# Performance work log

Hardware: AMD Instinct MI355X
Metric: run time of the kernel (lower is better)

## Reference

```python
import jax, jax.numpy as jnp
import numpy as np

B, T, C = 1, 2048, 1024
H = 16
HD = C // H  # 64
K = 8
EPS = 1e-6
NEG = -1.0e9


def apply_rotary_emb(x, cos, sin):
    # x: (B,T,H,HD), cos/sin: (T, HD//2)
    x1, x2 = jnp.split(x, 2, axis=-1)
    c = cos[None, :, None, :]
    s = sin[None, :, None, :]
    return jnp.concatenate([x1 * c - x2 * s, x1 * s + x2 * c], axis=-1)


def rms_norm(x):
    return x * jax.lax.rsqrt(jnp.mean(jnp.square(x), axis=-1, keepdims=True) + EPS)


def setup_inputs() -> dict:
    key = jax.random.key(0)
    ks = jax.random.split(key, 8)
    x = jax.random.normal(ks[0], (B, T, C), dtype=jnp.float32)
    # standard RoPE tables
    inv_freq = 1.0 / (10000.0 ** (np.arange(0, HD, 2, dtype=np.float32) / HD))
    t = np.arange(T, dtype=np.float32)
    freqs = np.outer(t, inv_freq)  # (T, HD//2)
    cos = jnp.asarray(np.cos(freqs), dtype=jnp.float32)
    sin = jnp.asarray(np.sin(freqs), dtype=jnp.float32)
    std = 0.02
    Wq = std * jax.random.normal(ks[1], (C, C), dtype=jnp.float32)
    Wk = std * jax.random.normal(ks[2], (C, C), dtype=jnp.float32)
    Wv = std * jax.random.normal(ks[3], (C, C), dtype=jnp.float32)
    Wproj = std * jax.random.normal(ks[4], (C, C), dtype=jnp.float32)
    Wdq = jax.random.normal(ks[5], (C, K), dtype=jnp.float32) / np.sqrt(C)
    Wdk = jax.random.normal(ks[6], (C, K), dtype=jnp.float32) / np.sqrt(C)
    return {"x": x, "cos": cos, "sin": sin, "Wq": Wq, "Wk": Wk, "Wv": Wv,
            "Wproj": Wproj, "Wdq": Wdq, "Wdk": Wdk}


def reference(x, cos, sin, Wq, Wk, Wv, Wproj, Wdq, Wdk):
    b, t, c = x.shape
    q = (x @ Wq).reshape(b, t, H, HD)
    k = (x @ Wk).reshape(b, t, H, HD)
    v = (x @ Wv).reshape(b, t, H, HD)
    q = rms_norm(apply_rotary_emb(q, cos, sin))
    k = rms_norm(apply_rotary_emb(k, cos, sin))

    # digit projections (identical for every head in the source module)
    qd = x @ Wdq  # (B,T,K)
    kd = x @ Wdk  # (B,T,K)
    matches = qd[:, :, None, :] == kd[:, None, :, :]  # (B,Tq,Tk,K)
    prefix = jnp.cumprod(matches.astype(jnp.int32), axis=-1)
    lcp = jnp.sum(prefix, axis=-1)  # (B,Tq,Tk)
    lcp_mask = lcp >= (K - 1)

    causal = jnp.tril(jnp.ones((t, t), dtype=bool))
    combined = causal[None, None, :, :] & lcp_mask[:, None, :, :]  # (B,1->H,Tq,Tk)

    scale = 1.0 / jnp.sqrt(jnp.asarray(HD, x.dtype))
    scores = jnp.einsum('bqhd,bkhd->bhqk', q * scale, k)
    scores = jnp.where(combined, scores, NEG)
    w = jax.nn.softmax(scores, axis=-1)
    y = jnp.einsum('bhqk,bkhd->bqhd', w, v).reshape(b, t, c)
    return y @ Wproj
```

## Files before the change

kernel.cpp:

```cpp
#include <hip/hip_runtime.h>
#include <math.h>

#define T_DIM 2048
#define C_DIM 1024
#define H_NUM 16
#define HD_DIM 64
#define K_LCP 8
#define NEG_VAL -1.0e9f

typedef __bf16 bf16;
typedef __bf16 bf16x4 __attribute__((ext_vector_type(4)));
typedef __bf16 bf16x8 __attribute__((ext_vector_type(8)));
typedef float f32x4 __attribute__((ext_vector_type(4)));

__device__ void matvec_body(const float* __restrict__ vin, int npart,
                            const float* __restrict__ W, float* __restrict__ vout,
                            float scale, int blk) {
  __shared__ float xm[C_DIM];
  __shared__ float red[4][64];
  const int t = threadIdx.x;
  f32x4 s = {0.f, 0.f, 0.f, 0.f};
  if (npart) {
    for (int g = 0; g < npart; ++g) s += ((const f32x4*)vin)[g * 256 + t];
  } else {
    s = ((const f32x4*)vin)[t];
  }
  s *= scale;
  *(f32x4*)&xm[t * 4] = s;
  __syncthreads();
  const int j = blk * 64 + (t & 63);
  const int p = t >> 6;
  float acc = 0.f;
  for (int c = p * 256; c < p * 256 + 256; ++c)
    acc = fmaf(xm[c], W[(size_t)c * C_DIM + j], acc);
  red[p][t & 63] = acc;
  __syncthreads();
  if (t < 64)
    vout[blk * 64 + t] = (red[0][t] + red[1][t]) + (red[2][t] + red[3][t]);
}

__global__ __launch_bounds__(256) void fused_a(const float* __restrict__ x,
                                               const float* __restrict__ Wdq,
                                               const float* __restrict__ Wdk,
                                               bf16* __restrict__ xb,
                                               float* __restrict__ qd,
                                               float* __restrict__ kd,
                                               float* __restrict__ partial,
                                               int* __restrict__ flags) {
  const int tid = threadIdx.x;
  if (blockIdx.x >= 512) {
    const int b = blockIdx.x - 512;
    if (b == 0 && tid < 116) flags[tid] = 0;
    f32x4 s = {0.f, 0.f, 0.f, 0.f};
    for (int r = 0; r < 64; ++r)
      s += ((const f32x4*)(x + (size_t)(b * 64 + r) * C_DIM))[tid];
    ((f32x4*)(partial + (size_t)b * C_DIM))[tid] = s;
    return;
  }
  const int wave = tid >> 6, lane = tid & 63;
  const int t = blockIdx.x * 4 + wave;
  const float* xp = x + (size_t)t * C_DIM;
  bf16* xbp = xb + (size_t)t * C_DIM;
  float aq[8] = {}, ak[8] = {};
#pragma unroll
  for (int i = 0; i < 16; ++i) {
    const int c = i * 64 + lane;
    float xv = xp[c];
    xbp[c] = (bf16)xv;
    float4 wq0 = *(const float4*)(Wdq + (size_t)c * K_LCP);
    float4 wq1 = *(const float4*)(Wdq + (size_t)c * K_LCP + 4);
    float4 wk0 = *(const float4*)(Wdk + (size_t)c * K_LCP);
    float4 wk1 = *(const float4*)(Wdk + (size_t)c * K_LCP + 4);
    aq[0] = fmaf(xv, wq0.x, aq[0]); aq[1] = fmaf(xv, wq0.y, aq[1]);
    aq[2] = fmaf(xv, wq0.z, aq[2]); aq[3] = fmaf(xv, wq0.w, aq[3]);
    aq[4] = fmaf(xv, wq1.x, aq[4]); aq[5] = fmaf(xv, wq1.y, aq[5]);
    aq[6] = fmaf(xv, wq1.z, aq[6]); aq[7] = fmaf(xv, wq1.w, aq[7]);
    ak[0] = fmaf(xv, wk0.x, ak[0]); ak[1] = fmaf(xv, wk0.y, ak[1]);
    ak[2] = fmaf(xv, wk0.z, ak[2]); ak[3] = fmaf(xv, wk0.w, ak[3]);
    ak[4] = fmaf(xv, wk1.x, ak[4]); ak[5] = fmaf(xv, wk1.y, ak[5]);
    ak[6] = fmaf(xv, wk1.z, ak[6]); ak[7] = fmaf(xv, wk1.w, ak[7]);
  }
#pragma unroll
  for (int j = 0; j < 8; ++j) {
#pragma unroll
    for (int off = 32; off >= 1; off >>= 1) {
      aq[j] += __shfl_xor(aq[j], off);
      ak[j] += __shfl_xor(ak[j], off);
    }
  }
  if (lane == 0) {
    *(float4*)(qd + (size_t)t * K_LCP) = make_float4(aq[0], aq[1], aq[2], aq[3]);
    *(float4*)(qd + (size_t)t * K_LCP + 4) = make_float4(aq[4], aq[5], aq[6], aq[7]);
    *(float4*)(kd + (size_t)t * K_LCP) = make_float4(ak[0], ak[1], ak[2], ak[3]);
    *(float4*)(kd + (size_t)t * K_LCP + 4) = make_float4(ak[4], ak[5], ak[6], ak[7]);
  }
}

__global__ __launch_bounds__(256) void fused_b(
    const float* __restrict__ qd, const float* __restrict__ kd,
    const float* __restrict__ partial, const float* __restrict__ Wv,
    int* __restrict__ tilemask, int* __restrict__ allmask,
    float* __restrict__ vmean, int* __restrict__ qneed, int* __restrict__ kneed,
    int* __restrict__ vneed, int* __restrict__ vtneed, int* __restrict__ pneed,
    int* __restrict__ wneed) {
  const int tid = threadIdx.x;
  if (blockIdx.x >= 128) {
    matvec_body(partial, 32, Wv, vmean, 1.0f / 2048.0f, blockIdx.x - 128);
    return;
  }
  const int qb = blockIdx.x;
  __shared__ float qds[16][K_LCP];
  __shared__ int tm[32];
  if (tid < 32) tm[tid] = 0;
  if (tid < 16 * K_LCP)
    qds[tid >> 3][tid & 7] = qd[(size_t)(qb * 16 + (tid >> 3)) * K_LCP + (tid & 7)];
  __syncthreads();
  for (int key = tid; key < T_DIM; key += 256) {
    float kv[K_LCP];
    *(float4*)&kv[0] = *(const float4*)(kd + (size_t)key * K_LCP);
    *(float4*)&kv[4] = *(const float4*)(kd + (size_t)key * K_LCP + 4);
    int any = 0;
#pragma unroll
    for (int ql = 0; ql < 16; ++ql) {
      int qg = qb * 16 + ql;
      if (key > qg) continue;
      int lcp = 0;
#pragma unroll
      for (int jj = 0; jj < K_LCP; ++jj) {
        if (qds[ql][jj] == kv[jj]) lcp++;
        else break;
      }
      if (lcp >= K_LCP - 1) any = 1;
    }
    if (any) tm[key >> 6] = 1;
  }
  __syncthreads();
  int anytm = 0;
#pragma unroll
  for (int i = 0; i < 32; ++i) anytm |= tm[i];
  if (tid < 32) tilemask[qb * 32 + tid] = tm[tid];
  if (tid == 0) allmask[qb] = !anytm;
  if (anytm) {
    if (tid < 32) {
      if (tm[tid]) {
        atomicOr(&kneed[tid >> 1], 1);
        atomicOr(&vneed[tid >> 1], 1);
      } else {
        atomicOr(&vtneed[tid], 1);
        atomicOr(&vneed[tid >> 1], 1);
      }
    }
    if (tid == 0) {
      atomicOr(&qneed[qb >> 3], 1);
      atomicOr(&pneed[qb >> 2], 1);
      atomicOr(&wneed[0], 1);
      atomicOr(&wneed[1], 1);
      atomicOr(&wneed[2], 1);
      atomicOr(&wneed[3], 1);
    }
  }
}

__global__ __launch_bounds__(256) void fused_e(
    const float* __restrict__ vmean, const float* __restrict__ WprojF,
    float* __restrict__ rowout, const float* __restrict__ W0,
    const float* __restrict__ W1, const float* __restrict__ W2,
    const float* __restrict__ W3, bf16* __restrict__ O0, bf16* __restrict__ O1,
    bf16* __restrict__ O2, bf16* __restrict__ O3, const int* __restrict__ wneed) {
  if (blockIdx.x < 16) {
    matvec_body(vmean, 0, WprojF, rowout, 1.0f, blockIdx.x);
    return;
  }
  const int idx = blockIdx.x - 16;
  const int z = idx >> 8;
  if (!wneed[z]) return;
  const float* W = (z == 0) ? W0 : (z == 1) ? W1 : (z == 2) ? W2 : W3;
  bf16* O = (z == 0) ? O0 : (z == 1) ? O1 : (z == 2) ? O2 : O3;
  __shared__ bf16 tile[64][65];
  const int rem = idx & 255;
  const int bk = (rem >> 4) * 64;
  const int bn = (rem & 15) * 64;
  const int r = threadIdx.x >> 2;
  const int c0 = (threadIdx.x & 3) * 16;
  const float* src = W + (size_t)(bk + r) * C_DIM + bn + c0;
#pragma unroll
  for (int t = 0; t < 16; t += 4) {
    float4 f = *(const float4*)(src + t);
    tile[r][c0 + t + 0] = (bf16)f.x;
    tile[r][c0 + t + 1] = (bf16)f.y;
    tile[r][c0 + t + 2] = (bf16)f.z;
    tile[r][c0 + t + 3] = (bf16)f.w;
  }
  __syncthreads();
  bf16* dst = O + (size_t)(bn + r) * C_DIM + bk + c0;
#pragma unroll
  for (int t = 0; t < 16; ++t) dst[t] = tile[c0 + t][r];
}

template <int TMt, int MI, int NA>
__global__ __launch_bounds__(256) void gemm_bf16(
    const bf16* __restrict__ A, const bf16* __restrict__ Bt0,
    const bf16* __restrict__ Bt1, const bf16* __restrict__ Bt2, void* C0,
    void* C1, void* C2, int N, int Kd, int bf16_out,
    const float* __restrict__ cosT, const float* __restrict__ sinT,
    const int* __restrict__ fq, const int* __restrict__ fk,
    const int* __restrict__ fv, float* __restrict__ vtsum,
    const float* __restrict__ rowout, int mode) {
  if (!mode && blockIdx.z == 1) {
    const int b = blockIdx.y * 8 + blockIdx.x;
    f32x4 v = ((const f32x4*)rowout)[threadIdx.x];
#pragma unroll
    for (int r = 0; r < 8; ++r) {
      const int row = b * 8 + r;
      if (fq[row >> 6]) continue;
      ((f32x4*)((float*)C0 + (size_t)row * C_DIM))[threadIdx.x] = v;
    }
    return;
  }
  if (mode) {
    const int* f = (blockIdx.z == 0) ? fq : (blockIdx.z == 1) ? fk : fv;
    if (!f[blockIdx.y]) return;
  } else {
    if (!fq[blockIdx.y]) return;
  }
  const bf16* Bt = (blockIdx.z == 0) ? Bt0 : (blockIdx.z == 1) ? Bt1 : Bt2;
  __shared__ __align__(16) bf16 As[TMt * 32];
  __shared__ __align__(16) bf16 Bs[128 * 32];
  const int tid = threadIdx.x;
  const int bm = blockIdx.y * TMt;
  const int bn = blockIdx.x * 128;
  const int wave = tid >> 6, lane = tid & 63;
  const int lr = lane >> 2;
  const int lc = (lane & 3) * 8;
  bf16* gA = (bf16*)(A + (size_t)(bm + wave * 16 * NA + lr) * Kd + lc);
  bf16* gB = (bf16*)(Bt + (size_t)(bn + wave * 32 + lr) * Kd + lc);
  bf16* lA = As + wave * 512 * NA;
  bf16* lB = Bs + wave * 1024;
  const int wr = (wave >> 1) * (MI * 16);
  const int wc = (wave & 1) * 64;
  const int fm = lane & 15;
  const int fk_ = (lane >> 4) * 8;

  f32x4 acc[MI][4] = {};
  for (int k0 = 0; k0 < Kd; k0 += 32) {
    __syncthreads();
#pragma unroll
    for (int u = 0; u < NA; ++u)
      __builtin_amdgcn_global_load_lds(
          (__attribute__((address_space(1))) void*)(gA + (size_t)u * 16 * Kd + k0),
          (__attribute__((address_space(3))) void*)(lA + u * 512), 16, 0, 0);
#pragma unroll
    for (int u = 0; u < 2; ++u)
      __builtin_amdgcn_global_load_lds(
          (__attribute__((address_space(1))) void*)(gB + (size_t)u * 16 * Kd + k0),
          (__attribute__((address_space(3))) void*)(lB + u * 512), 16, 0, 0);
    __syncthreads();
    bf16x8 af[MI], bfr[4];
#pragma unroll
    for (int i = 0; i < MI; ++i)
      af[i] = *(const bf16x8*)(As + (size_t)(wr + i * 16 + fm) * 32 + fk_);
#pragma unroll
    for (int j = 0; j < 4; ++j)
      bfr[j] = *(const bf16x8*)(Bs + (size_t)(wc + j * 16 + fm) * 32 + fk_);
#pragma unroll
    for (int i = 0; i < MI; ++i)
#pragma unroll
      for (int j = 0; j < 4; ++j)
        acc[i][j] = __builtin_amdgcn_mfma_f32_16x16x32_bf16(af[i], bfr[j],
                                                            acc[i][j], 0, 0, 0);
  }
  const int cq = (lane >> 4) * 4;
  if (mode && blockIdx.z < 2) {
    bf16* C = (bf16*)((blockIdx.z == 0) ? C0 : C1);
#pragma unroll
    for (int i = 0; i < MI; ++i)
#pragma unroll
      for (int r = 0; r < 4; ++r) {
        const int t = bm + wr + i * 16 + cq + r;
        float c0 = cosT[(size_t)t * 32 + fm], s0 = sinT[(size_t)t * 32 + fm];
        float c1 = cosT[(size_t)t * 32 + 16 + fm], s1 = sinT[(size_t)t * 32 + 16 + fm];
        float a0 = acc[i][0][r], a1 = acc[i][1][r];
        float a2 = acc[i][2][r], a3 = acc[i][3][r];
        float o0 = a0 * c0 - a2 * s0, o2 = a0 * s0 + a2 * c0;
        float o1 = a1 * c1 - a3 * s1, o3 = a1 * s1 + a3 * c1;
        float ss = o0 * o0 + o1 * o1 + o2 * o2 + o3 * o3;
        ss += __shfl_xor(ss, 1);
        ss += __shfl_xor(ss, 2);
        ss += __shfl_xor(ss, 4);
        ss += __shfl_xor(ss, 8);
        float rn = 1.0f / sqrtf(ss * (1.0f / 64.0f) + 1e-6f);
        size_t base = (size_t)t * N + bn + wc + fm;
        C[base + 0] = (bf16)(o0 * rn);
        C[base + 16] = (bf16)(o1 * rn);
        C[base + 32] = (bf16)(o2 * rn);
        C[base + 48] = (bf16)(o3 * rn);
      }
  } else if (bf16_out) {
    bf16* C = (bf16*)((blockIdx.z == 0) ? C0 : (blockIdx.z == 1) ? C1 : C2);
#pragma unroll
    for (int i = 0; i < MI; ++i)
#pragma unroll
      for (int r = 0; r < 4; ++r) {
        size_t base = (size_t)(bm + wr + i * 16 + cq + r) * N + bn + wc + fm;
#pragma unroll
        for (int j = 0; j < 4; ++j) C[base + j * 16] = (bf16)acc[i][j][r];
      }
    if (mode && blockIdx.z == 2 && MI == 4) {
      const int kt = (bm + wr) >> 6;
#pragma unroll
      for (int j = 0; j < 4; ++j) {
        float s = 0.f;
#pragma unroll
        for (int i = 0; i < MI; ++i)
#pragma unroll
          for (int r = 0; r < 4; ++r) s += acc[i][j][r];
        s += __shfl_xor(s, 16);
        s += __shfl_xor(s, 32);
        if ((lane >> 4) == 0)
          vtsum[(size_t)kt * C_DIM + bn + wc + j * 16 + fm] = s;
      }
    }
  } else {
    float* C = (float*)((blockIdx.z == 0) ? C0 : (blockIdx.z == 1) ? C1 : C2);
#pragma unroll
    for (int i = 0; i < MI; ++i)
#pragma unroll
      for (int r = 0; r < 4; ++r) {
        size_t base = (size_t)(bm + wr + i * 16 + cq + r) * N + bn + wc + fm;
#pragma unroll
        for (int j = 0; j < 4; ++j) C[base + j * 16] = acc[i][j][r];
      }
  }
}

#define QT 16
#define KT 64

__global__ __launch_bounds__(256) void attn2(
    const bf16* __restrict__ q, const bf16* __restrict__ k,
    const bf16* __restrict__ v, const float* __restrict__ qd,
    const float* __restrict__ kd, const float* __restrict__ vtsum,
    const float* __restrict__ vmean, const int* __restrict__ tilemask,
    const int* __restrict__ allmask, const int* __restrict__ pneed,
    bf16* __restrict__ y) {
  const int h = blockIdx.y;
  const int qb = blockIdx.x;
  const int q0 = qb * QT;
  const int tid = threadIdx.x;
  const int q_l = tid >> 4;
  const int sub = tid & 15;

  if (allmask[qb]) {
    if (pneed[qb >> 2]) {
      f32x4 vm = *(const f32x4*)(vmean + h * HD_DIM + sub * 4);
      bf16x4 o = {(bf16)vm[0], (bf16)vm[1], (bf16)vm[2], (bf16)vm[3]};
      *(bf16x4*)(y + (size_t)(q0 + q_l) * C_DIM + h * HD_DIM + sub * 4) = o;
    }
    return;
  }

  __shared__ float qs[QT][HD_DIM];
  __shared__ float qds[QT][K_LCP];
  __shared__ float ks[KT][HD_DIM];
  __shared__ float vs[KT][HD_DIM];
  __shared__ float kds[KT][K_LCP];
  __shared__ float sc[QT][KT + 4];

  {
    int r = tid >> 4, c4 = (tid & 15) * 4;
    bf16x4 t4 = *(const bf16x4*)(q + (size_t)(q0 + r) * C_DIM + h * HD_DIM + c4);
    qs[r][c4 + 0] = (float)t4[0] * 0.125f;
    qs[r][c4 + 1] = (float)t4[1] * 0.125f;
    qs[r][c4 + 2] = (float)t4[2] * 0.125f;
    qs[r][c4 + 3] = (float)t4[3] * 0.125f;
    if (tid < QT * K_LCP)
      qds[tid >> 3][tid & 7] = qd[(size_t)(q0 + (tid >> 3)) * K_LCP + (tid & 7)];
  }
  __syncthreads();

  float m = -INFINITY;
  float l = 0.f;
  float acc[4] = {0.f, 0.f, 0.f, 0.f};

  for (int kt = 0; kt < T_DIM / KT; ++kt) {
    if (!tilemask[qb * 32 + kt]) {
      if (m <= NEG_VAL) {
        m = NEG_VAL;
        l += (float)KT;
        f32x4 vt = *(const f32x4*)(vtsum + (size_t)kt * C_DIM + h * HD_DIM + sub * 4);
        acc[0] += vt[0];
        acc[1] += vt[1];
        acc[2] += vt[2];
        acc[3] += vt[3];
      }
      continue;
    }
    const int k0 = kt * KT;
    __syncthreads();
#pragma unroll
    for (int it = 0; it < 4; ++it) {
      int i = tid + it * 256;
      int row = i >> 4, c4 = (i & 15) * 4;
      bf16x4 kv = *(const bf16x4*)(k + (size_t)(k0 + row) * C_DIM + h * HD_DIM + c4);
      bf16x4 vv = *(const bf16x4*)(v + (size_t)(k0 + row) * C_DIM + h * HD_DIM + c4);
      ks[row][c4 + 0] = (float)kv[0];
      ks[row][c4 + 1] = (float)kv[1];
      ks[row][c4 + 2] = (float)kv[2];
      ks[row][c4 + 3] = (float)kv[3];
      vs[row][c4 + 0] = (float)vv[0];
      vs[row][c4 + 1] = (float)vv[1];
      vs[row][c4 + 2] = (float)vv[2];
      vs[row][c4 + 3] = (float)vv[3];
    }
#pragma unroll
    for (int it = 0; it < 2; ++it) {
      int i = tid + it * 256;
      kds[i >> 3][i & 7] = kd[(size_t)(k0 + (i >> 3)) * K_LCP + (i & 7)];
    }
    __syncthreads();

    const int kb = sub * 4;
    bool msk[4];
#pragma unroll
    for (int j = 0; j < 4; ++j) {
      int kg = k0 + kb + j;
      int lcp = 0;
#pragma unroll
      for (int jj = 0; jj < K_LCP; ++jj) {
        if (qds[q_l][jj] == kds[kb + j][jj]) lcp++;
        else break;
      }
      msk[j] = (lcp >= K_LCP - 1) && (kg <= q0 + q_l);
    }
    float s[4] = {0.f, 0.f, 0.f, 0.f};
#pragma unroll
    for (int d4 = 0; d4 < 16; ++d4) {
      float4 q4 = *(const float4*)&qs[q_l][d4 * 4];
#pragma unroll
      for (int j = 0; j < 4; ++j) {
        float4 k4 = *(const float4*)&ks[kb + j][d4 * 4];
        s[j] = fmaf(q4.x, k4.x, s[j]);
        s[j] = fmaf(q4.y, k4.y, s[j]);
        s[j] = fmaf(q4.z, k4.z, s[j]);
        s[j] = fmaf(q4.w, k4.w, s[j]);
      }
    }
    float tmax = NEG_VAL;
#pragma unroll
    for (int j = 0; j < 4; ++j) {
      s[j] = msk[j] ? s[j] : NEG_VAL;
      tmax = fmaxf(tmax, s[j]);
    }
#pragma unroll
    for (int off = 1; off < 16; off <<= 1) tmax = fmaxf(tmax, __shfl_xor(tmax, off));
    float m_new = fmaxf(m, tmax);
    float alpha = expf(m - m_new);
    float lsum = 0.f;
#pragma unroll
    for (int j = 0; j < 4; ++j) {
      float p = expf(s[j] - m_new);
      sc[q_l][kb + j] = p;
      lsum += p;
    }
#pragma unroll
    for (int off = 1; off < 16; off <<= 1) lsum += __shfl_xor(lsum, off);
    l = l * alpha + lsum;
    m = m_new;
    acc[0] *= alpha;
    acc[1] *= alpha;
    acc[2] *= alpha;
    acc[3] *= alpha;
    __syncthreads();
#pragma unroll 8
    for (int kk = 0; kk < KT; ++kk) {
      float w = sc[q_l][kk];
      const float4 v4 = *(const float4*)&vs[kk][sub * 4];
      acc[0] = fmaf(w, v4.x, acc[0]);
      acc[1] = fmaf(w, v4.y, acc[1]);
      acc[2] = fmaf(w, v4.z, acc[2]);
      acc[3] = fmaf(w, v4.w, acc[3]);
    }
  }

  const float inv_l = 1.0f / l;
  bf16x4 o = {(bf16)(acc[0] * inv_l), (bf16)(acc[1] * inv_l),
              (bf16)(acc[2] * inv_l), (bf16)(acc[3] * inv_l)};
  *(bf16x4*)(y + (size_t)(q0 + q_l) * C_DIM + h * HD_DIM + sub * 4) = o;
}

extern "C" void kernel_launch(void* const* d_in, const int* in_sizes, int n_in,
                              void* d_out, int out_size, void* d_ws, size_t ws_size,
                              hipStream_t stream) {
  const float* x = (const float*)d_in[0];
  const float* cosT = (const float*)d_in[1];
  const float* sinT = (const float*)d_in[2];
  const float* Wq = (const float*)d_in[3];
  const float* Wk = (const float*)d_in[4];
  const float* Wv = (const float*)d_in[5];
  const float* Wproj = (const float*)d_in[6];
  const float* Wdq = (const float*)d_in[7];
  const float* Wdk = (const float*)d_in[8];
  float* out = (float*)d_out;

  char* ws = (char*)d_ws;
  const size_t TC2 = (size_t)T_DIM * C_DIM * 2;
  const size_t CC2 = (size_t)C_DIM * C_DIM * 2;
  bf16* xb = (bf16*)(ws + 0);
  bf16* wqt = (bf16*)(ws + TC2);
  bf16* wkt = (bf16*)(ws + TC2 + CC2);
  bf16* wvt = (bf16*)(ws + TC2 + 2 * CC2);
  bf16* wpt = (bf16*)(ws + TC2 + 3 * CC2);
  bf16* qb = (bf16*)(ws + TC2 + 4 * CC2);
  bf16* kb = (bf16*)(ws + 2 * TC2 + 4 * CC2);
  bf16* vb = (bf16*)(ws + 3 * TC2 + 4 * CC2);
  char* p2 = ws + 4 * TC2 + 4 * CC2;
  float* qd = (float*)p2;                      p2 += (size_t)T_DIM * K_LCP * 4;
  float* kd = (float*)p2;                      p2 += (size_t)T_DIM * K_LCP * 4;
  float* vtsum = (float*)p2;                   p2 += 32 * C_DIM * 4;
  float* vmean = (float*)p2;                   p2 += C_DIM * 4;
  float* partial = (float*)p2;                 p2 += 32 * C_DIM * 4;
  float* rowout = (float*)p2;                  p2 += C_DIM * 4;
  int* tilemask = (int*)p2;                    p2 += (T_DIM / 16) * 32 * 4;
  int* allmask = (int*)p2;                     p2 += (T_DIM / 16) * 4;
  int* qneed = (int*)p2;                       p2 += 16 * 4;
  int* kneed = (int*)p2;                       p2 += 16 * 4;
  int* vneed = (int*)p2;                       p2 += 16 * 4;
  int* vtneed = (int*)p2;                      p2 += 32 * 4;
  int* pneed = (int*)p2;                       p2 += 32 * 4;
  int* wneed = (int*)p2;                       p2 += 4 * 4;
  bf16* yb = xb;

  fused_a<<<544, 256, 0, stream>>>(x, Wdq, Wdk, xb, qd, kd, partial, qneed);
  fused_b<<<144, 256, 0, stream>>>(qd, kd, partial, Wv, tilemask, allmask,
                                   vmean, qneed, kneed, vneed, vtneed, pneed,
                                   wneed);
  fused_e<<<16 + 1024, 256, 0, stream>>>(vmean, Wproj, rowout, Wq, Wk, Wv,
                                         Wproj, wqt, wkt, wvt, wpt, wneed);
  gemm_bf16<128, 4, 2><<<dim3(C_DIM / 128, T_DIM / 128, 3), 256, 0, stream>>>(
      xb, wqt, wkt, wvt, qb, kb, vb, C_DIM, C_DIM, 1, cosT, sinT, qneed, kneed,
      vneed, vtsum, rowout, 1);
  attn2<<<dim3(T_DIM / QT, H_NUM), 256, 0, stream>>>(
      qb, kb, vb, qd, kd, vtsum, vmean, tilemask, allmask, pneed, yb);
  gemm_bf16<64, 2, 1><<<dim3(C_DIM / 128, T_DIM / 64, 2), 256, 0, stream>>>(
      yb, wpt, wpt, wpt, out, out, out, C_DIM, C_DIM, 0, cosT, sinT, pneed,
      pneed, pneed, vtsum, rowout, 0);
}
```

Before: 121.6 us.

## Fuse all stages into one persistent kernel with grid-wide barriers

Replaces six separate kernel launches with a single persistent kernel of 256 blocks. Each stage runs as a grid-stride loop over virtual blocks, and the stages are separated by a custom atomic-based grid barrier. Shared memory is unified through a union. The goal is to remove launch overhead and inter-kernel gaps. The weight transposes are now always performed, where before they were gated by the wneed flags. In exchange it risks deadlock if not all blocks are co-resident, adds barrier spin cost, and reduces parallelism in stages that previously used many more blocks (1040, 2048).

```diff
diff --git a/kernel.cpp b/kernel.cpp
--- a/kernel.cpp
+++ b/kernel.cpp
@@ -7,70 +7,72 @@
 #define HD_DIM 64
 #define K_LCP 8
 #define NEG_VAL -1.0e9f
+#define SYNC_MAGIC 0x13579BDF
 
 typedef __bf16 bf16;
 typedef __bf16 bf16x4 __attribute__((ext_vector_type(4)));
 typedef __bf16 bf16x8 __attribute__((ext_vector_type(8)));
 typedef float f32x4 __attribute__((ext_vector_type(4)));
 
-__device__ void matvec_body(const float* __restrict__ vin, int npart,
-                            const float* __restrict__ W, float* __restrict__ vout,
-                            float scale, int blk) {
-  __shared__ float xm[C_DIM];
-  __shared__ float red[4][64];
-  const int t = threadIdx.x;
-  f32x4 s = {0.f, 0.f, 0.f, 0.f};
-  if (npart) {
-    for (int g = 0; g < npart; ++g) s += ((const f32x4*)vin)[g * 256 + t];
-  } else {
-    s = ((const f32x4*)vin)[t];
-  }
-  s *= scale;
-  *(f32x4*)&xm[t * 4] = s;
-  __syncthreads();
-  const int j = blk * 64 + (t & 63);
-  const int p = t >> 6;
-  float acc = 0.f;
-  for (int c = p * 256; c < p * 256 + 256; ++c)
-    acc = fmaf(xm[c], W[(size_t)c * C_DIM + j], acc);
-  red[p][t & 63] = acc;
-  __syncthreads();
-  if (t < 64)
-    vout[blk * 64 + t] = (red[0][t] + red[1][t]) + (red[2][t] + red[3][t]);
-}
-
-__global__ __launch_bounds__(256) void fused_a(const float* __restrict__ x,
-                                               const float* __restrict__ Wdq,
-                                               const float* __restrict__ Wdk,
-                                               bf16* __restrict__ xb,
-                                               float* __restrict__ qd,
-                                               float* __restrict__ kd,
-                                               float* __restrict__ partial,
-                                               int* __restrict__ flags) {
-  const int tid = threadIdx.x;
-  if (blockIdx.x >= 512) {
-    const int b = blockIdx.x - 512;
-    if (b == 0 && tid < 116) flags[tid] = 0;
-    f32x4 s = {0.f, 0.f, 0.f, 0.f};
-    for (int r = 0; r < 64; ++r)
-      s += ((const f32x4*)(x + (size_t)(b * 64 + r) * C_DIM))[tid];
-    ((f32x4*)(partial + (size_t)b * C_DIM))[tid] = s;
-    return;
-  }
-  const int wave = tid >> 6, lane = tid & 63;
-  const int t = blockIdx.x * 4 + wave;
-  const float* xp = x + (size_t)t * C_DIM;
-  bf16* xbp = xb + (size_t)t * C_DIM;
+struct Args {
+  const float *x, *cosT, *sinT, *Wq, *Wk, *Wv, *Wproj, *Wdq, *Wdk;
+  float* out;
+  bf16 *xb, *wqt, *wkt, *wvt, *wpt, *qB, *kB, *vB;
+  float *qd, *kd, *vtsum, *vmean, *partial, *rowout;
+  int *tilemask, *allmask, *qneed, *kneed, *vneed, *vtneed, *pneed;
+  int* sync;
+};
+
+union SmemU {
+  struct {
+    float qs[16][64]; float qds[16][8]; float ks[64][64]; float vs[64][64];
+    float kds[64][8]; float sc[16][68];
+  } attn;
+  struct { bf16 As[128 * 32]; bf16 Bs[128 * 32]; } gemm;
+  struct { bf16 tile[64][65]; } tp;
+  struct { float xm[C_DIM]; float red[4][64]; } mv;
+  struct { float qds[16][8]; int tm[32]; } tmask;
+};
+
+__device__ void gsync(int* s, int nb) {
+  __syncthreads();
+  if (threadIdx.x == 0) {
+    __threadfence();
+    int g = __hip_atomic_load(&s[2], __ATOMIC_RELAXED, __HIP_MEMORY_SCOPE_AGENT);
+    int old = __hip_atomic_fetch_add(&s[1], 1, __ATOMIC_ACQ_REL,
+                                     __HIP_MEMORY_SCOPE_AGENT);
+    if (old == nb - 1) {
+      __hip_atomic_store(&s[1], 0, __ATOMIC_RELAXED, __HIP_MEMORY_SCOPE_AGENT);
+      __hip_atomic_store(&s[2], g + 1, __ATOMIC_RELEASE,
+                         __HIP_MEMORY_SCOPE_AGENT);
+    } else {
+      int it = 0;
+      while (__hip_atomic_load(&s[2], __ATOMIC_ACQUIRE,
+                               __HIP_MEMORY_SCOPE_AGENT) == g) {
+        __builtin_amdgcn_s_sleep(2);
+        if (++it > (1 << 25)) break;
+      }
+    }
+    __threadfence();
+  }
+  __syncthreads();
+}
+
+__device__ void conv_qdkd_body(const Args& a, int vb) {
+  const int wave = threadIdx.x >> 6, lane = threadIdx.x & 63;
+  const int t = vb * 4 + wave;
+  const float* xp = a.x + (size_t)t * C_DIM;
+  bf16* xbp = a.xb + (size_t)t * C_DIM;
   float aq[8] = {}, ak[8] = {};
 #pragma unroll
   for (int i = 0; i < 16; ++i) {
     const int c = i * 64 + lane;
     float xv = xp[c];
     xbp[c] = (bf16)xv;
-    float4 wq0 = *(const float4*)(Wdq + (size_t)c * K_LCP);
-    float4 wq1 = *(const float4*)(Wdq + (size_t)c * K_LCP + 4);
-    float4 wk0 = *(const float4*)(Wdk + (size_t)c * K_LCP);
-    float4 wk1 = *(const float4*)(Wdk + (size_t)c * K_LCP + 4);
+    float4 wq0 = *(const float4*)(a.Wdq + (size_t)c * K_LCP);
+    float4 wq1 = *(const float4*)(a.Wdq + (size_t)c * K_LCP + 4);
+    float4 wk0 = *(const float4*)(a.Wdk + (size_t)c * K_LCP);
+    float4 wk1 = *(const float4*)(a.Wdk + (size_t)c * K_LCP + 4);
     aq[0] = fmaf(xv, wq0.x, aq[0]); aq[1] = fmaf(xv, wq0.y, aq[1]);
     aq[2] = fmaf(xv, wq0.z, aq[2]); aq[3] = fmaf(xv, wq0.w, aq[3]);
     aq[4] = fmaf(xv, wq1.x, aq[4]); aq[5] = fmaf(xv, wq1.y, aq[5]);
@@ -89,146 +91,133 @@
     }
   }
   if (lane == 0) {
-    *(float4*)(qd + (size_t)t * K_LCP) = make_float4(aq[0], aq[1], aq[2], aq[3]);
-    *(float4*)(qd + (size_t)t * K_LCP + 4) = make_float4(aq[4], aq[5], aq[6], aq[7]);
-    *(float4*)(kd + (size_t)t * K_LCP) = make_float4(ak[0], ak[1], ak[2], ak[3]);
-    *(float4*)(kd + (size_t)t * K_LCP + 4) = make_float4(ak[4], ak[5], ak[6], ak[7]);
-  }
-}
-
-__global__ __launch_bounds__(256) void fused_b(
-    const float* __restrict__ qd, const float* __restrict__ kd,
-    const float* __restrict__ partial, const float* __restrict__ Wv,
-    int* __restrict__ tilemask, int* __restrict__ allmask,
-    float* __restrict__ vmean, int* __restrict__ qneed, int* __restrict__ kneed,
-    int* __restrict__ vneed, int* __restrict__ vtneed, int* __restrict__ pneed,
-    int* __restrict__ wneed) {
-  const int tid = threadIdx.x;
-  if (blockIdx.x >= 128) {
-    matvec_body(partial, 32, Wv, vmean, 1.0f / 2048.0f, blockIdx.x - 128);
-    return;
-  }
-  const int qb = blockIdx.x;
-  __shared__ float qds[16][K_LCP];
-  __shared__ int tm[32];
-  if (tid < 32) tm[tid] = 0;
-  if (tid < 16 * K_LCP)
-    qds[tid >> 3][tid & 7] = qd[(size_t)(qb * 16 + (tid >> 3)) * K_LCP + (tid & 7)];
-  __syncthreads();
-  for (int key = tid; key < T_DIM; key += 256) {
-    float kv[K_LCP];
-    *(float4*)&kv[0] = *(const float4*)(kd + (size_t)key * K_LCP);
-    *(float4*)&kv[4] = *(const float4*)(kd + (size_t)key * K_LCP + 4);
-    int any = 0;
-#pragma unroll
-    for (int ql = 0; ql < 16; ++ql) {
-      int qg = qb * 16 + ql;
-      if (key > qg) continue;
-      int lcp = 0;
-#pragma unroll
-      for (int jj = 0; jj < K_LCP; ++jj) {
-        if (qds[ql][jj] == kv[jj]) lcp++;
-        else break;
-      }
-      if (lcp >= K_LCP - 1) any = 1;
-    }
-    if (any) tm[key >> 6] = 1;
-  }
-  __syncthreads();
-  int anytm = 0;
-#pragma unroll
-  for (int i = 0; i < 32; ++i) anytm |= tm[i];
-  if (tid < 32) tilemask[qb * 32 + tid] = tm[tid];
-  if (tid == 0) allmask[qb] = !anytm;
-  if (anytm) {
-    if (tid < 32) {
-      if (tm[tid]) {
-        atomicOr(&kneed[tid >> 1], 1);
-        atomicOr(&vneed[tid >> 1], 1);
-      } else {
-        atomicOr(&vtneed[tid], 1);
-        atomicOr(&vneed[tid >> 1], 1);
-      }
-    }
-    if (tid == 0) {
-      atomicOr(&qneed[qb >> 3], 1);
-      atomicOr(&pneed[qb >> 2], 1);
-      atomicOr(&wneed[0], 1);
-      atomicOr(&wneed[1], 1);
-      atomicOr(&wneed[2], 1);
-      atomicOr(&wneed[3], 1);
-    }
-  }
-}
-
-__global__ __launch_bounds__(256) void fused_e(
-    const float* __restrict__ vmean, const float* __restrict__ WprojF,
-    float* __restrict__ rowout, const float* __restrict__ W0,
-    const float* __restrict__ W1, const float* __restrict__ W2,
-    const float* __restrict__ W3, bf16* __restrict__ O0, bf16* __restrict__ O1,
-    bf16* __restrict__ O2, bf16* __restrict__ O3, const int* __restrict__ wneed) {
-  if (blockIdx.x < 16) {
-    matvec_body(vmean, 0, WprojF, rowout, 1.0f, blockIdx.x);
-    return;
-  }
-  const int idx = blockIdx.x - 16;
+    *(float4*)(a.qd + (size_t)t * K_LCP) = make_float4(aq[0], aq[1], aq[2], aq[3]);
+    *(float4*)(a.qd + (size_t)t * K_LCP + 4) = make_float4(aq[4], aq[5], aq[6], aq[7]);
+    *(float4*)(a.kd + (size_t)t * K_LCP) = make_float4(ak[0], ak[1], ak[2], ak[3]);
+    *(float4*)(a.kd + (size_t)t * K_LCP + 4) = make_float4(ak[4], ak[5], ak[6], ak[7]);
+  }
+}
+
+__device__ void xpartial_body(const Args& a, int b) {
+  const int t = threadIdx.x;
+  f32x4 s = {0.f, 0.f, 0.f, 0.f};
+  for (int r = 0; r < 64; ++r)
+    s += ((const f32x4*)(a.x + (size_t)(b * 64 + r) * C_DIM))[t];
+  ((f32x4*)(a.partial + (size_t)b * C_DIM))[t] = s;
+}
+
+__device__ void transpose_body(SmemU& sm, const Args& a, int idx) {
   const int z = idx >> 8;
-  if (!wneed[z]) return;
-  const float* W = (z == 0) ? W0 : (z == 1) ? W1 : (z == 2) ? W2 : W3;
-  bf16* O = (z == 0) ? O0 : (z == 1) ? O1 : (z == 2) ? O2 : O3;
-  __shared__ bf16 tile[64][65];
+  const float* W = (z == 0) ? a.Wq : (z == 1) ? a.Wk : (z == 2) ? a.Wv : a.Wproj;
+  bf16* O = (z == 0) ? a.wqt : (z == 1) ? a.wkt : (z == 2) ? a.wvt : a.wpt;
   const int rem = idx & 255;
   const int bk = (rem >> 4) * 64;
   const int bn = (rem & 15) * 64;
   const int r = threadIdx.x >> 2;
   const int c0 = (threadIdx.x & 3) * 16;
+  __syncthreads();
   const float* src = W + (size_t)(bk + r) * C_DIM + bn + c0;
 #pragma unroll
   for (int t = 0; t < 16; t += 4) {
     float4 f = *(const float4*)(src + t);
-    tile[r][c0 + t + 0] = (bf16)f.x;
-    tile[r][c0 + t + 1] = (bf16)f.y;
-    tile[r][c0 + t + 2] = (bf16)f.z;
-    tile[r][c0 + t + 3] = (bf16)f.w;
+    sm.tp.tile[r][c0 + t + 0] = (bf16)f.x;
+    sm.tp.tile[r][c0 + t + 1] = (bf16)f.y;
+    sm.tp.tile[r][c0 + t + 2] = (bf16)f.z;
+    sm.tp.tile[r][c0 + t + 3] = (bf16)f.w;
   }
   __syncthreads();
   bf16* dst = O + (size_t)(bn + r) * C_DIM + bk + c0;
 #pragma unroll
-  for (int t = 0; t < 16; ++t) dst[t] = tile[c0 + t][r];
+  for (int t = 0; t < 16; ++t) dst[t] = sm.tp.tile[c0 + t][r];
+}
+
+__device__ void tilemask_body(SmemU& sm, const Args& a, int qb) {
+  const int tid = threadIdx.x;
+  __syncthreads();
+  if (tid < 32) sm.tmask.tm[tid] = 0;
+  if (tid < 16 * K_LCP)
+    sm.tmask.qds[tid >> 3][tid & 7] =
+        a.qd[(size_t)(qb * 16 + (tid >> 3)) * K_LCP + (tid & 7)];
+  __syncthreads();
+  for (int key = tid; key < T_DIM; key += 256) {
+    float kv[K_LCP];
+    *(float4*)&kv[0] = *(const float4*)(a.kd + (size_t)key * K_LCP);
+    *(float4*)&kv[4] = *(const float4*)(a.kd + (size_t)key * K_LCP + 4);
+    int any = 0;
+#pragma unroll
+    for (int ql = 0; ql < 16; ++ql) {
+      int qg = qb * 16 + ql;
+      if (key > qg) continue;
+      int lcp = 0;
+#pragma unroll
+      for (int jj = 0; jj < K_LCP; ++jj) {
+        if (sm.tmask.qds[ql][jj] == kv[jj]) lcp++;
+        else break;
+      }
+      if (lcp >= K_LCP - 1) any = 1;
+    }
+    if (any) sm.tmask.tm[key >> 6] = 1;
+  }
+  __syncthreads();
+  int anytm = 0;
+#pragma unroll
+  for (int i = 0; i < 32; ++i) anytm |= sm.tmask.tm[i];
+  if (tid < 32) a.tilemask[qb * 32 + tid] = sm.tmask.tm[tid];
+  if (tid == 0) a.allmask[qb] = !anytm;
+  if (anytm) {
+    if (tid < 32) {
+      if (sm.tmask.tm[tid]) {
+        atomicOr(&a.kneed[tid >> 1], 1);
+        atomicOr(&a.vneed[tid >> 1], 1);
+      } else {
+        atomicOr(&a.vtneed[tid], 1);
+        atomicOr(&a.vneed[tid >> 1], 1);
+      }
+    }
+    if (tid == 0) {
+      atomicOr(&a.qneed[qb >> 3], 1);
+      atomicOr(&a.pneed[qb >> 2], 1);
+    }
+  }
+  __syncthreads();
+}
+
+__device__ void matvec_body(SmemU& sm, const float* vin, int npart,
+                            const float* W, float* vout, float scale, int blk) {
+  const int t = threadIdx.x;
+  __syncthreads();
+  f32x4 s = {0.f, 0.f, 0.f, 0.f};
+  if (npart) {
+    for (int g = 0; g < npart; ++g) s += ((const f32x4*)vin)[g * 256 + t];
+  } else {
+    s = ((const f32x4*)vin)[t];
+  }
+  s *= scale;
+  *(f32x4*)&sm.mv.xm[t * 4] = s;
+  __syncthreads();
+  const int j = blk * 64 + (t & 63);
+  const int p = t >> 6;
+  float acc = 0.f;
+  for (int c = p * 256; c < p * 256 + 256; ++c)
+    acc = fmaf(sm.mv.xm[c], W[(size_t)c * C_DIM + j], acc);
+  sm.mv.red[p][t & 63] = acc;
+  __syncthreads();
+  if (t < 64)
+    vout[blk * 64 + t] =
+        (sm.mv.red[0][t] + sm.mv.red[1][t]) + (sm.mv.red[2][t] + sm.mv.red[3][t]);
+  __syncthreads();
 }
 
 template <int TMt, int MI, int NA>
-__global__ __launch_bounds__(256) void gemm_bf16(
-    const bf16* __restrict__ A, const bf16* __restrict__ Bt0,
-    const bf16* __restrict__ Bt1, const bf16* __restrict__ Bt2, void* C0,
-    void* C1, void* C2, int N, int Kd, int bf16_out,
-    const float* __restrict__ cosT, const float* __restrict__ sinT,
-    const int* __restrict__ fq, const int* __restrict__ fk,
-    const int* __restrict__ fv, float* __restrict__ vtsum,
-    const float* __restrict__ rowout, int mode) {
-  if (!mode && blockIdx.z == 1) {
-    const int b = blockIdx.y * 8 + blockIdx.x;
-    f32x4 v = ((const f32x4*)rowout)[threadIdx.x];
-#pragma unroll
-    for (int r = 0; r < 8; ++r) {
-      const int row = b * 8 + r;
-      if (fq[row >> 6]) continue;
-      ((f32x4*)((float*)C0 + (size_t)row * C_DIM))[threadIdx.x] = v;
-    }
-    return;
-  }
-  if (mode) {
-    const int* f = (blockIdx.z == 0) ? fq : (blockIdx.z == 1) ? fk : fv;
-    if (!f[blockIdx.y]) return;
-  } else {
-    if (!fq[blockIdx.y]) return;
-  }
-  const bf16* Bt = (blockIdx.z == 0) ? Bt0 : (blockIdx.z == 1) ? Bt1 : Bt2;
-  __shared__ __align__(16) bf16 As[TMt * 32];
-  __shared__ __align__(16) bf16 Bs[128 * 32];
+__device__ void gemm_body(SmemU& sm, const Args& a, const bf16* A,
+                          const bf16* Bt, void* Cv, int bx, int by, int z,
+                          int mode) {
+  bf16* As = sm.gemm.As;
+  bf16* Bs = sm.gemm.Bs;
   const int tid = threadIdx.x;
-  const int bm = blockIdx.y * TMt;
-  const int bn = blockIdx.x * 128;
+  const int Kd = C_DIM, N = C_DIM;
+  const int bm = by * TMt;
+  const int bn = bx * 128;
   const int wave = tid >> 6, lane = tid & 63;
   const int lr = lane >> 2;
   const int lc = (lane & 3) * 8;
@@ -253,7 +242,7 @@
     for (int u = 0; u < 2; ++u)
       __builtin_amdgcn_global_load_lds(
           (__attribute__((address_space(1))) void*)(gB + (size_t)u * 16 * Kd + k0),
-          (__attribute__((address_space(3))) void*)(lB + u * 512), 16, 0, 0);
+          (__attribute__((address_space(3))) void*)(lB + u * 1024 / 2), 16, 0, 0);
     __syncthreads();
     bf16x8 af[MI], bfr[4];
 #pragma unroll
@@ -269,16 +258,18 @@
         acc[i][j] = __builtin_amdgcn_mfma_f32_16x16x32_bf16(af[i], bfr[j],
                                                             acc[i][j], 0, 0, 0);
   }
+  __syncthreads();
   const int cq = (lane >> 4) * 4;
-  if (mode && blockIdx.z < 2) {
-    bf16* C = (bf16*)((blockIdx.z == 0) ? C0 : C1);
+  if (mode && z < 2) {
+    bf16* C = (bf16*)Cv;
 #pragma unroll
     for (int i = 0; i < MI; ++i)
 #pragma unroll
       for (int r = 0; r < 4; ++r) {
         const int t = bm + wr + i * 16 + cq + r;
-        float c0 = cosT[(size_t)t * 32 + fm], s0 = sinT[(size_t)t * 32 + fm];
-        float c1 = cosT[(size_t)t * 32 + 16 + fm], s1 = sinT[(size_t)t * 32 + 16 + fm];
+        float c0 = a.cosT[(size_t)t * 32 + fm], s0 = a.sinT[(size_t)t * 32 + fm];
+        float c1 = a.cosT[(size_t)t * 32 + 16 + fm];
+        float s1 = a.sinT[(size_t)t * 32 + 16 + fm];
         float a0 = acc[i][0][r], a1 = acc[i][1][r];
         float a2 = acc[i][2][r], a3 = acc[i][3][r];
         float o0 = a0 * c0 - a2 * s0, o2 = a0 * s0 + a2 * c0;
@@ -295,8 +286,8 @@
         C[base + 32] = (bf16)(o2 * rn);
         C[base + 48] = (bf16)(o3 * rn);
       }
-  } else if (bf16_out) {
-    bf16* C = (bf16*)((blockIdx.z == 0) ? C0 : (blockIdx.z == 1) ? C1 : C2);
+  } else if (mode) {
+    bf16* C = (bf16*)Cv;
 #pragma unroll
     for (int i = 0; i < MI; ++i)
 #pragma unroll
@@ -305,23 +296,21 @@
 #pragma unroll
         for (int j = 0; j < 4; ++j) C[base + j * 16] = (bf16)acc[i][j][r];
       }
-    if (mode && blockIdx.z == 2 && MI == 4) {
-      const int kt = (bm + wr) >> 6;
-#pragma unroll
-      for (int j = 0; j < 4; ++j) {
-        float s = 0.f;
-#pragma unroll
-        for (int i = 0; i < MI; ++i)
-#pragma unroll
-          for (int r = 0; r < 4; ++r) s += acc[i][j][r];
-        s += __shfl_xor(s, 16);
-        s += __shfl_xor(s, 32);
-        if ((lane >> 4) == 0)
-          vtsum[(size_t)kt * C_DIM + bn + wc + j * 16 + fm] = s;
-      }
+    const int kt = (bm + wr) >> 6;
+#pragma unroll
+    for (int j = 0; j < 4; ++j) {
+      float s = 0.f;
+#pragma unroll
+      for (int i = 0; i < MI; ++i)
+#pragma unroll
+        for (int r = 0; r < 4; ++r) s += acc[i][j][r];
+      s += __shfl_xor(s, 16);
+      s += __shfl_xor(s, 32);
+      if ((lane >> 4) == 0)
+        a.vtsum[(size_t)kt * C_DIM + bn + wc + j * 16 + fm] = s;
     }
   } else {
-    float* C = (float*)((blockIdx.z == 0) ? C0 : (blockIdx.z == 1) ? C1 : C2);
+    float* C = (float*)Cv;
 #pragma unroll
     for (int i = 0; i < MI; ++i)
 #pragma unroll
@@ -333,48 +322,32 @@
   }
 }
 
-#define QT 16
-#define KT 64
-
-__global__ __launch_bounds__(256) void attn2(
-    const bf16* __restrict__ q, const bf16* __restrict__ k,
-    const bf16* __restrict__ v, const float* __restrict__ qd,
-    const float* __restrict__ kd, const float* __restrict__ vtsum,
-    const float* __restrict__ vmean, const int* __restrict__ tilemask,
-    const int* __restrict__ allmask, const int* __restrict__ pneed,
-    bf16* __restrict__ y) {
-  const int h = blockIdx.y;
-  const int qb = blockIdx.x;
-  const int q0 = qb * QT;
+__device__ void attn_body(SmemU& sm, const Args& a, int qb, int h) {
+  const int q0 = qb * 16;
   const int tid = threadIdx.x;
   const int q_l = tid >> 4;
   const int sub = tid & 15;
 
-  if (allmask[qb]) {
-    if (pneed[qb >> 2]) {
-      f32x4 vm = *(const f32x4*)(vmean + h * HD_DIM + sub * 4);
+  if (a.allmask[qb]) {
+    if (a.pneed[qb >> 2]) {
+      f32x4 vm = *(const f32x4*)(a.vmean + h * HD_DIM + sub * 4);
       bf16x4 o = {(bf16)vm[0], (bf16)vm[1], (bf16)vm[2], (bf16)vm[3]};
-      *(bf16x4*)(y + (size_t)(q0 + q_l) * C_DIM + h * HD_DIM + sub * 4) = o;
+      *(bf16x4*)(a.xb + (size_t)(q0 + q_l) * C_DIM + h * HD_DIM + sub * 4) = o;
     }
     return;
   }
 
-  __shared__ float qs[QT][HD_DIM];
-  __shared__ float qds[QT][K_LCP];
-  __shared__ float ks[KT][HD_DIM];
-  __shared__ float vs[KT][HD_DIM];
-  __shared__ float kds[KT][K_LCP];
-  __shared__ float sc[QT][KT + 4];
-
+  __syncthreads();
   {
     int r = tid >> 4, c4 = (tid & 15) * 4;
-    bf16x4 t4 = *(const bf16x4*)(q + (size_t)(q0 + r) * C_DIM + h * HD_DIM + c4);
-    qs[r][c4 + 0] = (float)t4[0] * 0.125f;
-    qs[r][c4 + 1] = (float)t4[1] * 0.125f;
-    qs[r][c4 + 2] = (float)t4[2] * 0.125f;
-    qs[r][c4 + 3] = (float)t4[3] * 0.125f;
-    if (tid < QT * K_LCP)
-      qds[tid >> 3][tid & 7] = qd[(size_t)(q0 + (tid >> 3)) * K_LCP + (tid & 7)];
+    bf16x4 t4 = *(const bf16x4*)(a.qB + (size_t)(q0 + r) * C_DIM + h * HD_DIM + c4);
+    sm.attn.qs[r][c4 + 0] = (float)t4[0] * 0.125f;
+    sm.attn.qs[r][c4 + 1] = (float)t4[1] * 0.125f;
+    sm.attn.qs[r][c4 + 2] = (float)t4[2] * 0.125f;
+    sm.attn.qs[r][c4 + 3] = (float)t4[3] * 0.125f;
+    if (tid < 16 * K_LCP)
+      sm.attn.qds[tid >> 3][tid & 7] =
+          a.qd[(size_t)(q0 + (tid >> 3)) * K_LCP + (tid & 7)];
   }
   __syncthreads();
 
@@ -382,40 +355,40 @@
   float l = 0.f;
   float acc[4] = {0.f, 0.f, 0.f, 0.f};
 
-  for (int kt = 0; kt < T_DIM / KT; ++kt) {
-    if (!tilemask[qb * 32 + kt]) {
+  for (int kt = 0; kt < 32; ++kt) {
+    if (!a.tilemask[qb * 32 + kt]) {
       if (m <= NEG_VAL) {
         m = NEG_VAL;
-        l += (float)KT;
-        f32x4 vt = *(const f32x4*)(vtsum + (size_t)kt * C_DIM + h * HD_DIM + sub * 4);
-        acc[0] += vt[0];
-        acc[1] += vt[1];
-        acc[2] += vt[2];
-        acc[3] += vt[3];
+        l += 64.0f;
+        f32x4 vt =
+            *(const f32x4*)(a.vtsum + (size_t)kt * C_DIM + h * HD_DIM + sub * 4);
+        acc[0] += vt[0]; acc[1] += vt[1]; acc[2] += vt[2]; acc[3] += vt[3];
       }
       continue;
     }
-    const int k0 = kt * KT;
+    const int k0 = kt * 64;
     __syncthreads();
 #pragma unroll
     for (int it = 0; it < 4; ++it) {
       int i = tid + it * 256;
       int row = i >> 4, c4 = (i & 15) * 4;
-      bf16x4 kv = *(const bf16x4*)(k + (size_t)(k0 + row) * C_DIM + h * HD_DIM + c4);
-      bf16x4 vv = *(const bf16x4*)(v + (size_t)(k0 + row) * C_DIM + h * HD_DIM + c4);
-      ks[row][c4 + 0] = (float)kv[0];
-      ks[row][c4 + 1] = (float)kv[1];
-      ks[row][c4 + 2] = (float)kv[2];
-      ks[row][c4 + 3] = (float)kv[3];
-      vs[row][c4 + 0] = (float)vv[0];
-      vs[row][c4 + 1] = (float)vv[1];
-      vs[row][c4 + 2] = (float)vv[2];
-      vs[row][c4 + 3] = (float)vv[3];
+      bf16x4 kv =
+          *(const bf16x4*)(a.kB + (size_t)(k0 + row) * C_DIM + h * HD_DIM + c4);
+      bf16x4 vv =
+          *(const bf16x4*)(a.vB + (size_t)(k0 + row) * C_DIM + h * HD_DIM + c4);
+      sm.attn.ks[row][c4 + 0] = (float)kv[0];
+      sm.attn.ks[row][c4 + 1] = (float)kv[1];
+      sm.attn.ks[row][c4 + 2] = (float)kv[2];
+      sm.attn.ks[row][c4 + 3] = (float)kv[3];
+      sm.attn.vs[row][c4 + 0] = (float)vv[0];
+      sm.attn.vs[row][c4 + 1] = (float)vv[1];
+      sm.attn.vs[row][c4 + 2] = (float)vv[2];
+      sm.attn.vs[row][c4 + 3] = (float)vv[3];
     }
 #pragma unroll
     for (int it = 0; it < 2; ++it) {
       int i = tid + it * 256;
-      kds[i >> 3][i & 7] = kd[(size_t)(k0 + (i >> 3)) * K_LCP + (i & 7)];
+      sm.attn.kds[i >> 3][i & 7] = a.kd[(size_t)(k0 + (i >> 3)) * K_LCP + (i & 7)];
     }
     __syncthreads();
 
@@ -427,7 +400,7 @@
       int lcp = 0;
 #pragma unroll
       for (int jj = 0; jj < K_LCP; ++jj) {
-        if (qds[q_l][jj] == kds[kb + j][jj]) lcp++;
+        if (sm.attn.qds[q_l][jj] == sm.attn.kds[kb + j][jj]) lcp++;
         else break;
       }
       msk[j] = (lcp >= K_LCP - 1) && (kg <= q0 + q_l);
@@ -435,10 +408,10 @@
     float s[4] = {0.f, 0.f, 0.f, 0.f};
 #pragma unroll
     for (int d4 = 0; d4 < 16; ++d4) {
-      float4 q4 = *(const float4*)&qs[q_l][d4 * 4];
+      float4 q4 = *(const float4*)&sm.attn.qs[q_l][d4 * 4];
 #pragma unroll
       for (int j = 0; j < 4; ++j) {
-        float4 k4 = *(const float4*)&ks[kb + j][d4 * 4];
+        float4 k4 = *(const float4*)&sm.attn.ks[kb + j][d4 * 4];
         s[j] = fmaf(q4.x, k4.x, s[j]);
         s[j] = fmaf(q4.y, k4.y, s[j]);
         s[j] = fmaf(q4.z, k4.z, s[j]);
@@ -459,22 +432,19 @@
 #pragma unroll
     for (int j = 0; j < 4; ++j) {
       float p = expf(s[j] - m_new);
-      sc[q_l][kb + j] = p;
+      sm.attn.sc[q_l][kb + j] = p;
       lsum += p;
     }
 #pragma unroll
     for (int off = 1; off < 16; off <<= 1) lsum += __shfl_xor(lsum, off);
     l = l * alpha + lsum;
     m = m_new;
-    acc[0] *= alpha;
-    acc[1] *= alpha;
-    acc[2] *= alpha;
-    acc[3] *= alpha;
+    acc[0] *= alpha; acc[1] *= alpha; acc[2] *= alpha; acc[3] *= alpha;
     __syncthreads();
 #pragma unroll 8
-    for (int kk = 0; kk < KT; ++kk) {
-      float w = sc[q_l][kk];
-      const float4 v4 = *(const float4*)&vs[kk][sub * 4];
+    for (int kk = 0; kk < 64; ++kk) {
+      float w = sm.attn.sc[q_l][kk];
+      const float4 v4 = *(const float4*)&sm.attn.vs[kk][sub * 4];
       acc[0] = fmaf(w, v4.x, acc[0]);
       acc[1] = fmaf(w, v4.y, acc[1]);
       acc[2] = fmaf(w, v4.z, acc[2]);
@@ -485,63 +455,131 @@
   const float inv_l = 1.0f / l;
   bf16x4 o = {(bf16)(acc[0] * inv_l), (bf16)(acc[1] * inv_l),
               (bf16)(acc[2] * inv_l), (bf16)(acc[3] * inv_l)};
-  *(bf16x4*)(y + (size_t)(q0 + q_l) * C_DIM + h * HD_DIM + sub * 4) = o;
+  *(bf16x4*)(a.xb + (size_t)(q0 + q_l) * C_DIM + h * HD_DIM + sub * 4) = o;
+  __syncthreads();
+}
+
+__device__ void bcast_body(const Args& a, int b) {
+  f32x4 v = ((const f32x4*)a.rowout)[threadIdx.x];
+#pragma unroll
+  for (int r = 0; r < 8; ++r) {
+    const int row = b * 8 + r;
+    if (a.pneed[row >> 6]) continue;
+    ((f32x4*)(a.out + (size_t)row * C_DIM))[threadIdx.x] = v;
+  }
+}
+
+__global__ __launch_bounds__(256, 1) void mega(Args a) {
+  const int nb = gridDim.x;
+  __shared__ SmemU sm;
+
+  if (blockIdx.x == 0 && threadIdx.x == 0) {
+    __hip_atomic_store(&a.sync[1], 0, __ATOMIC_RELAXED, __HIP_MEMORY_SCOPE_AGENT);
+    __hip_atomic_store(&a.sync[2], 0, __ATOMIC_RELAXED, __HIP_MEMORY_SCOPE_AGENT);
+    __hip_atomic_store(&a.sync[0], SYNC_MAGIC, __ATOMIC_RELEASE,
+                       __HIP_MEMORY_SCOPE_AGENT);
+  }
+  if (threadIdx.x == 0) {
+    int it = 0;
+    while (__hip_atomic_load(&a.sync[0], __ATOMIC_ACQUIRE,
+                             __HIP_MEMORY_SCOPE_AGENT) != SYNC_MAGIC) {
+      __builtin_amdgcn_s_sleep(2);
+      if (++it > (1 << 25)) break;
+    }
+  }
+  __syncthreads();
+
+  for (int vb = blockIdx.x; vb < 1568; vb += nb) {
+    if (vb < 512) {
+      conv_qdkd_body(a, vb);
+    } else if (vb < 544) {
+      if (vb == 512 && threadIdx.x < 116) a.qneed[threadIdx.x] = 0;
+      xpartial_body(a, vb - 512);
+    } else {
+      transpose_body(sm, a, vb - 544);
+    }
+  }
+  gsync(a.sync, nb);
+
+  for (int vb = blockIdx.x; vb < 144; vb += nb) {
+    if (vb < 128)
+      tilemask_body(sm, a, vb);
+    else
+      matvec_body(sm, a.partial, 32, a.Wv, a.vmean, 1.0f / 2048.0f, vb - 128);
+  }
+  gsync(a.sync, nb);
+
+  for (int vb = blockIdx.x; vb < 400; vb += nb) {
+    if (vb < 384) {
+      int z = vb >> 7, r = vb & 127, by = r >> 3, bx = r & 7;
+      const int* f = (z == 0) ? a.qneed : (z == 1) ? a.kneed : a.vneed;
+      if (f[by]) {
+        const bf16* Bt = (z == 0) ? a.wqt : (z == 1) ? a.wkt : a.wvt;
+        void* C = (z == 0) ? (void*)a.qB : (z == 1) ? (void*)a.kB : (void*)a.vB;
+        gemm_body<128, 4, 2>(sm, a, a.xb, Bt, C, bx, by, z, 1);
+      }
+    } else {
+      matvec_body(sm, a.vmean, 0, a.Wproj, a.rowout, 1.0f, vb - 384);
+    }
+  }
+  gsync(a.sync, nb);
+
+  for (int vb = blockIdx.x; vb < 2048; vb += nb)
+    attn_body(sm, a, vb >> 4, vb & 15);
+  gsync(a.sync, nb);
+
+  for (int vb = blockIdx.x; vb < 512; vb += nb) {
+    if (vb < 256) {
+      int by = vb >> 3, bx = vb & 7;
+      if (a.pneed[by])
+        gemm_body<64, 2, 1>(sm, a, a.xb, a.wpt, (void*)a.out, bx, by, 0, 0);
+    } else {
+      bcast_body(a, vb - 256);
+    }
+  }
 }
 
 extern "C" void kernel_launch(void* const* d_in, const int* in_sizes, int n_in,
                               void* d_out, int out_size, void* d_ws, size_t ws_size,
                               hipStream_t stream) {
-  const float* x = (const float*)d_in[0];
-  const float* cosT = (const float*)d_in[1];
-  const float* sinT = (const float*)d_in[2];
-  const float* Wq = (const float*)d_in[3];
-  const float* Wk = (const float*)d_in[4];
-  const float* Wv = (const float*)d_in[5];
-  const float* Wproj = (const float*)d_in[6];
-  const float* Wdq = (const float*)d_in[7];
-  const float* Wdk = (const float*)d_in[8];
-  float* out = (float*)d_out;
-
   char* ws = (char*)d_ws;
   const size_t TC2 = (size_t)T_DIM * C_DIM * 2;
   const size_t CC2 = (size_t)C_DIM * C_DIM * 2;
-  bf16* xb = (bf16*)(ws + 0);
-  bf16* wqt = (bf16*)(ws + TC2);
-  bf16* wkt = (bf16*)(ws + TC2 + CC2);
-  bf16* wvt = (bf16*)(ws + TC2 + 2 * CC2);
-  bf16* wpt = (bf16*)(ws + TC2 + 3 * CC2);
-  bf16* qb = (bf16*)(ws + TC2 + 4 * CC2);
-  bf16* kb = (bf16*)(ws + 2 * TC2 + 4 * CC2);
-  bf16* vb = (bf16*)(ws + 3 * TC2 + 4 * CC2);
+
+  Args a;
+  a.x = (const float*)d_in[0];
+  a.cosT = (const float*)d_in[1];
+  a.sinT = (const float*)d_in[2];
+  a.Wq = (const float*)d_in[3];
+  a.Wk = (const float*)d_in[4];
+  a.Wv = (const float*)d_in[5];
+  a.Wproj = (const float*)d_in[6];
+  a.Wdq = (const float*)d_in[7];
+  a.Wdk = (const float*)d_in[8];
+  a.out = (float*)d_out;
+  a.xb = (bf16*)(ws + 0);
+  a.wqt = (bf16*)(ws + TC2);
+  a.wkt = (bf16*)(ws + TC2 + CC2);
+  a.wvt = (bf16*)(ws + TC2 + 2 * CC2);
+  a.wpt = (bf16*)(ws + TC2 + 3 * CC2);
+  a.qB = (bf16*)(ws + TC2 + 4 * CC2);
+  a.kB = (bf16*)(ws + 2 * TC2 + 4 * CC2);
+  a.vB = (bf16*)(ws + 3 * TC2 + 4 * CC2);
   char* p2 = ws + 4 * TC2 + 4 * CC2;
-  float* qd = (float*)p2;                      p2 += (size_t)T_DIM * K_LCP * 4;
-  float* kd = (float*)p2;                      p2 += (size_t)T_DIM * K_LCP * 4;
-  float* vtsum = (float*)p2;                   p2 += 32 * C_DIM * 4;
-  float* vmean = (float*)p2;                   p2 += C_DIM * 4;
-  float* partial = (float*)p2;                 p2 += 32 * C_DIM * 4;
-  float* rowout = (float*)p2;                  p2 += C_DIM * 4;
-  int* tilemask = (int*)p2;                    p2 += (T_DIM / 16) * 32 * 4;
-  int* allmask = (int*)p2;                     p2 += (T_DIM / 16) * 4;
-  int* qneed = (int*)p2;                       p2 += 16 * 4;
-  int* kneed = (int*)p2;                       p2 += 16 * 4;
-  int* vneed = (int*)p2;                       p2 += 16 * 4;
-  int* vtneed = (int*)p2;                      p2 += 32 * 4;
-  int* pneed = (int*)p2;                       p2 += 32 * 4;
-  int* wneed = (int*)p2;                       p2 += 4 * 4;
-  bf16* yb = xb;
-
-  fused_a<<<544, 256, 0, stream>>>(x, Wdq, Wdk, xb, qd, kd, partial, qneed);
-  fused_b<<<144, 256, 0, stream>>>(qd, kd, partial, Wv, tilemask, allmask,
-                                   vmean, qneed, kneed, vneed, vtneed, pneed,
-                                   wneed);
-  fused_e<<<16 + 1024, 256, 0, stream>>>(vmean, Wproj, rowout, Wq, Wk, Wv,
-                                         Wproj, wqt, wkt, wvt, wpt, wneed);
-  gemm_bf16<128, 4, 2><<<dim3(C_DIM / 128, T_DIM / 128, 3), 256, 0, stream>>>(
-      xb, wqt, wkt, wvt, qb, kb, vb, C_DIM, C_DIM, 1, cosT, sinT, qneed, kneed,
-      vneed, vtsum, rowout, 1);
-  attn2<<<dim3(T_DIM / QT, H_NUM), 256, 0, stream>>>(
-      qb, kb, vb, qd, kd, vtsum, vmean, tilemask, allmask, pneed, yb);
-  gemm_bf16<64, 2, 1><<<dim3(C_DIM / 128, T_DIM / 64, 2), 256, 0, stream>>>(
-      yb, wpt, wpt, wpt, out, out, out, C_DIM, C_DIM, 0, cosT, sinT, pneed,
-      pneed, pneed, vtsum, rowout, 0);
-}
+  a.qd = (float*)p2;        p2 += (size_t)T_DIM * K_LCP * 4;
+  a.kd = (float*)p2;        p2 += (size_t)T_DIM * K_LCP * 4;
+  a.vtsum = (float*)p2;     p2 += 32 * C_DIM * 4;
+  a.vmean = (float*)p2;     p2 += C_DIM * 4;
+  a.partial = (float*)p2;   p2 += 32 * C_DIM * 4;
+  a.rowout = (float*)p2;    p2 += C_DIM * 4;
+  a.tilemask = (int*)p2;    p2 += (T_DIM / 16) * 32 * 4;
+  a.allmask = (int*)p2;     p2 += (T_DIM / 16) * 4;
+  a.qneed = (int*)p2;       p2 += 16 * 4;
+  a.kneed = (int*)p2;       p2 += 16 * 4;
+  a.vneed = (int*)p2;       p2 += 16 * 4;
+  a.vtneed = (int*)p2;      p2 += 32 * 4;
+  a.pneed = (int*)p2;       p2 += 32 * 4;
+  a.sync = (int*)p2;        p2 += 4 * 4;
+
+  mega<<<dim3(256), dim3(256), 0, stream>>>(a);
+}
```

Result: slower. 284.6 us (+134.1%).
